# Performance work log

Hardware: AMD Instinct MI355X
Metric: run time of the kernel (lower is better)

The kernel has to match this reference:

```python
import jax, jax.numpy as jnp
import numpy as np

RADIUS = 1.3
COARSE = 32          # coarse_reso
FINE = 2             # fine_reso[0]
NUM_ATOMS = 32
SH_DIM = 9           # (sh_deg+1)^2, sh_deg=2
DATA_DIM = SH_DIM * 3 + 1  # 28
BATCH = 512
N_INT = COARSE * 3 * 2 * FINE  # 384 intersections per ray

# 8 trilinear neighbor offsets, same order as the torch module
_OFFSETS = jnp.array([[-1, -1, -1], [-1, -1, 1], [-1, 1, -1], [-1, 1, 1],
                      [1, -1, -1], [1, -1, 1], [1, 1, -1], [1, 1, 1]], dtype=jnp.float32)


def sh_encode(d):
    """Real spherical harmonics basis, degree 2 (9 components), on normalized dirs."""
    d = d / jnp.linalg.norm(d, axis=-1, keepdims=True)
    x, y, z = d[..., 0], d[..., 1], d[..., 2]
    c0 = 0.28209479177387814
    c1 = 0.48860251190291987
    c2a = 1.0925484305920792
    c2b = 0.31539156525252005
    c2c = 0.5462742152960396
    return jnp.stack([
        c0 * jnp.ones_like(x),
        -c1 * y, c1 * z, -c1 * x,
        c2a * x * y, -c2a * y * z,
        c2b * (2.0 * z * z - x * x - y * y),
        -c2a * x * z,
        c2c * (x * x - y * y)], axis=-1)


def dict_interp(pts, grid, atoms):
    """Multi-res voxel trilinear gather + dictionary-atom accumulate.
    pts: [N,3] world coords; grid: [COARSE^3, A]; atoms: [FINE^3, A, D]."""
    fine_vlen = (2.0 * RADIUS / COARSE) / FINE
    p = (pts + RADIUS) / fine_vlen                       # [N,3] fine-grid coords
    pre = p[:, None, :] + _OFFSETS[None] / 2.0           # [N,8,3]
    post = jnp.clip(jnp.floor(pre), 0.0, COARSE * FINE - 1)
    offs = jnp.abs(p[:, None, :] - (post + 0.5))         # [N,8,3]
    w = jnp.prod(1.0 - offs, axis=-1)                    # [N,8] trilinear weights
    idx = post.astype(jnp.int32)
    c = idx // FINE                                      # coarse cell per-axis
    f = idx % FINE                                       # fine cell per-axis
    cflat = (c[..., 0] * COARSE + c[..., 1]) * COARSE + c[..., 2]  # [N,8]
    fflat = (f[..., 0] * FINE + f[..., 1]) * FINE + f[..., 2]      # [N,8]
    out = jnp.zeros((pts.shape[0], DATA_DIM), pts.dtype)
    for n in range(8):
        cv = grid[cflat[:, n]]                           # [N,A] gathered coarse weights
        av = atoms[fflat[:, n]]                          # [N,A,D] gathered atoms
        out = out + w[:, n, None] * jnp.einsum('na,nad->nd', cv, av)
    return out


def setup_inputs() -> dict:
    key = jax.random.key(0)
    k1, k2, k3, k4 = jax.random.split(key, 4)
    rays_o = jax.random.uniform(k1, (BATCH, 3), jnp.float32, -0.5, 0.5)
    rays_d = jax.random.normal(k2, (BATCH, 3), jnp.float32)
    rays_d = rays_d / jnp.linalg.norm(rays_d, axis=-1, keepdims=True)
    grid = 0.01 * jax.random.normal(k3, (COARSE ** 3, NUM_ATOMS), jnp.float32)
    atoms = jnp.concatenate([
        jax.random.uniform(k4, (FINE ** 3, NUM_ATOMS, DATA_DIM - 1), jnp.float32),
        jnp.full((FINE ** 3, NUM_ATOMS, 1), 0.01, jnp.float32)], axis=-1)
    return {"rays_o": rays_o, "rays_d": rays_d, "grid": grid, "atoms": atoms, "grid_id": 0}


def reference(rays_o, rays_d, grid, atoms, grid_id):
    del grid_id  # single scene
    step = ((2.0 * RADIUS / COARSE) / FINE) / 2.0
    # sample_proposal (no_grad in the original)
    off_pos = (RADIUS - rays_o) / rays_d
    off_neg = (-RADIUS - rays_o) / rays_d
    start = jnp.max(jnp.minimum(off_pos, off_neg), axis=-1, keepdims=True)
    steps = jnp.arange(N_INT, dtype=rays_o.dtype)[None]
    intersections = jax.lax.stop_gradient(start + steps * step)  # [B, N_INT]
    ts = intersections[:, :-1]                                    # [B, S]
    pts = jax.lax.stop_gradient(
        rays_o[:, None, :] + ts[..., None] * rays_d[:, None, :])  # [B,S,3]
    mask = jnp.all((pts > -RADIUS) & (pts < RADIUS), axis=-1)     # [B,S]
    B, S = ts.shape
    data = dict_interp(pts.reshape(-1, 3), grid, atoms).reshape(B, S, DATA_DIM)
    # masked_scatter_ equivalent: zero out out-of-box samples
    sigma = jnp.where(mask, jax.nn.relu(data[..., -1]), 0.0)
    dists = (intersections[:, 1:] - intersections[:, :-1]) * jnp.linalg.norm(rays_d, axis=-1, keepdims=True)
    alpha = 1.0 - jnp.exp(-sigma * dists)
    T = jnp.cumprod(1.0 - alpha + 1e-10, axis=-1)
    T = jnp.concatenate([jnp.ones_like(T[:, :1]), T[:, :-1]], axis=-1)
    abs_light = alpha * T                                         # [B,S]
    sh = sh_encode(rays_d)                                        # [B,SH_DIM]
    sh_vals = data[..., :-1].reshape(B, S, 3, SH_DIM)
    rgb_s = jnp.einsum('bk,bsck->bsc', sh, sh_vals)               # [B,S,3]
    rgb_s = jnp.where(mask[..., None], rgb_s, 0.0)
    rgb = jnp.sum(abs_light[..., None] * jax.nn.sigmoid(rgb_s), axis=1)
    rgb = rgb + (1.0 - jnp.sum(abs_light, axis=-1, keepdims=True))  # white background
    depth = jnp.sum(abs_light * ts, axis=-1)
    consistency_loss = jnp.zeros((), rgb.dtype)  # noise_std == 0
    return rgb, alpha, depth, consistency_loss
```

## Files before the change

### kernel.cpp

```cpp
#include <hip/hip_runtime.h>
#include <math.h>

#define R_ 1.3f
#define NCOARSE 32
#define SAMPLES 383
#define BATCH 512
#define STEPSZ 0.0203125f
#define INV_FINE_VLEN 24.615384615384617f

using f32x4 = __attribute__((ext_vector_type(4))) float;
using s16x8 = __attribute__((ext_vector_type(8))) short;
using u32x4 = __attribute__((ext_vector_type(4))) unsigned int;
using bf16x2 = __attribute__((ext_vector_type(2))) __bf16;

__device__ __forceinline__ unsigned int packbf2(float lo, float hi) {
    bf16x2 v;
    v.x = (__bf16)lo;
    v.y = (__bf16)hi;
    return __builtin_bit_cast(unsigned int, v);
}

__device__ __forceinline__ void dimwc(float p, float* W, int* C) {
    float post0 = fminf(fmaxf(floorf(p - 0.5f), 0.f), 63.f);
    float post1 = fminf(fmaxf(floorf(p + 0.5f), 0.f), 63.f);
    float w0 = 1.f - fabsf(p - (post0 + 0.5f));
    float w1 = 1.f - fabsf(p - (post1 + 0.5f));
    int i0 = (int)post0, i1 = (int)post1;
    int f0 = i0 & 1, f1 = i1 & 1;
    W[0] = (f0 == 0 ? w0 : 0.f) + (f1 == 0 ? w1 : 0.f);
    W[1] = (f0 == 1 ? w0 : 0.f) + (f1 == 1 ? w1 : 0.f);
    int c0 = i0 >> 1, c1 = i1 >> 1;
    C[0] = (f0 == 0) ? c0 : c1;
    C[1] = (f0 == 1) ? c0 : c1;
}

__global__ __launch_bounds__(512, 4) void dp_fused(
    const float* __restrict__ rays_o, const float* __restrict__ rays_d,
    const float* __restrict__ grid, const float* __restrict__ atoms,
    float* __restrict__ out_rgb, float* __restrict__ out_alpha,
    float* __restrict__ out_depth, float* __restrict__ out_loss)
{
    __shared__ u32x4 Bf[16][64];
    __shared__ float Dw[8][544];
    __shared__ float alpha_l[384];
    __shared__ float sig_l[384][3];
    __shared__ float segtot[8];
    __shared__ float part[6][5];

    const int b = blockIdx.x;
    const int tid = threadIdx.x;
    const int wid = tid >> 6, l = tid & 63;
    const int sl = l & 15, j8 = (l >> 4) * 8;

    const int s0i = tid, s1i = tid + 512;
    const int ll0 = s0i & 63, nt0 = (s0i >> 6) & 1, kb0 = s0i >> 7;
    const int ll1 = s1i & 63, nt1 = (s1i >> 6) & 1, kb1 = s1i >> 7;
    const int a00 = (ll0 >> 4) * 8, d0 = nt0 * 16 + (ll0 & 15);
    const int a01 = (ll1 >> 4) * 8, d1 = nt1 * 16 + (ll1 & 15);
    float la0[8], la1[8];
#pragma unroll
    for (int j = 0; j < 8; ++j) {
        la0[j] = (d0 < 28) ? atoms[(kb0 * 32 + a00 + j) * 28 + d0] : 0.f;
        la1[j] = (d1 < 28) ? atoms[(kb1 * 32 + a01 + j) * 28 + d1] : 0.f;
    }

    if (b == 0 && tid == 0) out_loss[0] = 0.f;

    if (tid < 384) alpha_l[tid] = 0.f;
    {
        float* sf = &sig_l[0][0];
        for (int i = tid; i < 384 * 3; i += 512) sf[i] = 0.f;
    }

    const float ox = rays_o[3 * b], oy = rays_o[3 * b + 1], oz = rays_o[3 * b + 2];
    const float dx = rays_d[3 * b], dy = rays_d[3 * b + 1], dz = rays_d[3 * b + 2];
    const float start = fmaxf(fmaxf(
        fminf((R_ - ox) / dx, (-R_ - ox) / dx),
        fminf((R_ - oy) / dy, (-R_ - oy) / dy)),
        fminf((R_ - oz) / dz, (-R_ - oz) / dz));
    const float t_exit = fminf(fminf(
        fmaxf((R_ - ox) / dx, (-R_ - ox) / dx),
        fmaxf((R_ - oy) / dy, (-R_ - oy) / dy)),
        fmaxf((R_ - oz) / dz, (-R_ - oz) / dz));
    const int ns = (int)floorf((t_exit - start) / STEPSZ) + 2;
    const int ntiles = min(24, (ns >> 4) + 2);

    const float lend = sqrtf(dx * dx + dy * dy + dz * dz);
    const float dist = STEPSZ * lend;
    const float inv = 1.f / lend;
    const float nx = dx * inv, ny = dy * inv, nz = dz * inv;
    float sh[9];
    sh[0] = 0.28209479177387814f;
    sh[1] = -0.48860251190291987f * ny;
    sh[2] = 0.48860251190291987f * nz;
    sh[3] = -0.48860251190291987f * nx;
    sh[4] = 1.0925484305920792f * nx * ny;
    sh[5] = -1.0925484305920792f * ny * nz;
    sh[6] = 0.31539156525252005f * (2.f * nz * nz - nx * nx - ny * ny);
    sh[7] = -1.0925484305920792f * nx * nz;
    sh[8] = 0.5462742152960396f * (nx * nx - ny * ny);

    {
        u32x4 o0, o1;
#pragma unroll
        for (int e2 = 0; e2 < 4; ++e2) {
            o0[e2] = packbf2(la0[2 * e2], la0[2 * e2 + 1]);
            o1[e2] = packbf2(la1[2 * e2], la1[2 * e2 + 1]);
        }
        Bf[s0i >> 6][ll0] = o0;
        Bf[s1i >> 6][ll1] = o1;
    }

    __syncthreads();

    float* Dbuf = &Dw[wid][0];

    for (int t = wid; t < ntiles; t += 8) {
        const int s = t * 16 + sl;
        const float tt = start + s * STEPSZ;
        const float px = ox + tt * dx, py = oy + tt * dy, pz = oz + tt * dz;
        const bool m = (s < SAMPLES) &&
                       (px > -R_ && px < R_ && py > -R_ && py < R_ && pz > -R_ && pz < R_);
        if (__ballot(m) == 0ull) continue;

        float W0[2], W1[2], W2[2];
        int C0[2], C1[2], C2[2];
        dimwc((px + R_) * INV_FINE_VLEN, W0, C0);
        dimwc((py + R_) * INV_FINE_VLEN, W1, C1);
        dimwc((pz + R_) * INV_FINE_VLEN, W2, C2);
        const float msk = m ? 1.f : 0.f;

        f32x4 acc0 = {0.f, 0.f, 0.f, 0.f};
        f32x4 acc1 = {0.f, 0.f, 0.f, 0.f};

#pragma unroll
        for (int half = 0; half < 2; ++half) {
            f32x4 qa[4], qb[4];
            float wf[4];
#pragma unroll
            for (int k2 = 0; k2 < 4; ++k2) {
                const int kb = half * 4 + k2;
                const int fx = (kb >> 2) & 1, fy = (kb >> 1) & 1, fz = kb & 1;
                wf[k2] = msk * W0[fx] * W1[fy] * W2[fz];
                const int cf = (C0[fx] * NCOARSE + C1[fy]) * NCOARSE + C2[fz];
                const f32x4* gp = (const f32x4*)(grid + cf * 32 + j8);
                qa[k2] = gp[0];
                qb[k2] = gp[1];
            }
#pragma unroll
            for (int k2 = 0; k2 < 4; ++k2) {
                const int kb = half * 4 + k2;
                const float w = wf[k2];
                u32x4 o;
                o.x = packbf2(w * qa[k2].x, w * qa[k2].y);
                o.y = packbf2(w * qa[k2].z, w * qa[k2].w);
                o.z = packbf2(w * qb[k2].x, w * qb[k2].y);
                o.w = packbf2(w * qb[k2].z, w * qb[k2].w);
                const s16x8 af = __builtin_bit_cast(s16x8, o);
                acc0 = __builtin_amdgcn_mfma_f32_16x16x32_bf16(
                    af, __builtin_bit_cast(s16x8, Bf[kb * 2 + 0][l]), acc0, 0, 0, 0);
                acc1 = __builtin_amdgcn_mfma_f32_16x16x32_bf16(
                    af, __builtin_bit_cast(s16x8, Bf[kb * 2 + 1][l]), acc1, 0, 0, 0);
            }
        }

        const int fp = l >> 4;
#pragma unroll
        for (int r = 0; r < 4; ++r) {
            Dbuf[(4 * fp + r) * 33 + sl]      = acc0[r];
            Dbuf[(4 * fp + r) * 33 + sl + 16] = acc1[r];
        }

        const int s2 = l >> 2, c = l & 3;
        const int so = t * 16 + s2;
        if (c == 3) {
            const float sigma = fmaxf(Dbuf[s2 * 33 + 27], 0.f);
            alpha_l[so] = 1.f - __expf(-sigma * dist);
        } else {
            float r_ = 0.f;
#pragma unroll
            for (int k = 0; k < 9; ++k) r_ += sh[k] * Dbuf[s2 * 33 + c * 9 + k];
            sig_l[so][c] = __builtin_amdgcn_rcpf(1.f + __expf(-r_));
        }
    }

    __syncthreads();

    if (tid < SAMPLES) out_alpha[b * SAMPLES + tid] = alpha_l[tid];

    float a_s = 0.f, incl = 1.f;
    if (wid < 6) {
        const int s = wid * 64 + l;
        const bool v = s < SAMPLES;
        a_s = v ? alpha_l[s] : 0.f;
        incl = v ? (1.f - a_s + 1e-10f) : 1.f;
#pragma unroll
        for (int off = 1; off < 64; off <<= 1) {
            const float tm = __shfl_up(incl, off, 64);
            if (l >= off) incl *= tm;
        }
        if (l == 63) segtot[wid] = incl;
    }
    __syncthreads();
    if (wid < 6) {
        float pre = 1.f;
        for (int k = 0; k < wid; ++k) pre *= segtot[k];
        float excl = __shfl_up(incl, 1, 64);
        if (l == 0) excl = 1.f;
        const int s = wid * 64 + l;
        const bool v = s < SAMPLES;
        const float al = v ? a_s * pre * excl : 0.f;
        float r0 = al * sig_l[s][0];
        float r1 = al * sig_l[s][1];
        float r2 = al * sig_l[s][2];
        float sd = al * (start + s * STEPSZ);
        float sa = al;
#pragma unroll
        for (int m2 = 32; m2 > 0; m2 >>= 1) {
            r0 += __shfl_xor(r0, m2, 64);
            r1 += __shfl_xor(r1, m2, 64);
            r2 += __shfl_xor(r2, m2, 64);
            sd += __shfl_xor(sd, m2, 64);
            sa += __shfl_xor(sa, m2, 64);
        }
        if (l == 0) {
            part[wid][0] = r0; part[wid][1] = r1; part[wid][2] = r2;
            part[wid][3] = sd; part[wid][4] = sa;
        }
    }
    __syncthreads();
    if (tid == 0) {
        float r0 = 0.f, r1 = 0.f, r2 = 0.f, sd = 0.f, sa = 0.f;
#pragma unroll
        for (int j = 0; j < 6; ++j) {
            r0 += part[j][0]; r1 += part[j][1]; r2 += part[j][2];
            sd += part[j][3]; sa += part[j][4];
        }
        const float base = 1.f - sa;
        out_rgb[b * 3 + 0] = r0 + base;
        out_rgb[b * 3 + 1] = r1 + base;
        out_rgb[b * 3 + 2] = r2 + base;
        out_depth[b] = sd;
    }
}

extern "C" void kernel_launch(void* const* d_in, const int* in_sizes, int n_in,
                              void* d_out, int out_size, void* d_ws, size_t ws_size,
                              hipStream_t stream) {
    const float* rays_o = (const float*)d_in[0];
    const float* rays_d = (const float*)d_in[1];
    const float* grid   = (const float*)d_in[2];
    const float* atoms  = (const float*)d_in[3];
    float* out   = (float*)d_out;
    float* rgb   = out;
    float* alpha = out + BATCH * 3;
    float* depth = out + BATCH * 3 + BATCH * SAMPLES;
    float* loss  = out + BATCH * 3 + BATCH * SAMPLES + BATCH;

    dp_fused<<<dim3(BATCH), dim3(512), 0, stream>>>(
        rays_o, rays_d, grid, atoms, rgb, alpha, depth, loss);
}
```

Baseline: 16.99 us.

## Software-pipeline grid gathers across tiles and prefetch before atom barrier

Replaces the per-wave tile loop with an explicitly unrolled, software-pipelined sequence of up to three tiles. The first half of each tile's grid gathers is issued early: the first tile's loads go out before the atom-packing barrier, and the next tile's loads go out while the current tile's MFMAs run. This aims to hide global gather latency. It also drops the per-tile early-skip ballot for fully masked tiles and moves the SH coefficients into shared memory, computed by one thread. That lowers register pressure but adds LDS reads in the epilogue.

```diff
diff --git a/kernel.cpp b/kernel.cpp
--- a/kernel.cpp
+++ b/kernel.cpp
@@ -44,6 +44,7 @@
     __shared__ float Dw[8][544];
     __shared__ float alpha_l[384];
     __shared__ float sig_l[384][3];
+    __shared__ float sh_s[9];
     __shared__ float segtot[8];
     __shared__ float part[6][5];
 
@@ -87,90 +88,73 @@
 
     const float lend = sqrtf(dx * dx + dy * dy + dz * dz);
     const float dist = STEPSZ * lend;
-    const float inv = 1.f / lend;
-    const float nx = dx * inv, ny = dy * inv, nz = dz * inv;
-    float sh[9];
-    sh[0] = 0.28209479177387814f;
-    sh[1] = -0.48860251190291987f * ny;
-    sh[2] = 0.48860251190291987f * nz;
-    sh[3] = -0.48860251190291987f * nx;
-    sh[4] = 1.0925484305920792f * nx * ny;
-    sh[5] = -1.0925484305920792f * ny * nz;
-    sh[6] = 0.31539156525252005f * (2.f * nz * nz - nx * nx - ny * ny);
-    sh[7] = -1.0925484305920792f * nx * nz;
-    sh[8] = 0.5462742152960396f * (nx * nx - ny * ny);
-
-    {
-        u32x4 o0, o1;
-#pragma unroll
-        for (int e2 = 0; e2 < 4; ++e2) {
-            o0[e2] = packbf2(la0[2 * e2], la0[2 * e2 + 1]);
-            o1[e2] = packbf2(la1[2 * e2], la1[2 * e2 + 1]);
-        }
-        Bf[s0i >> 6][ll0] = o0;
-        Bf[s1i >> 6][ll1] = o1;
-    }
-
-    __syncthreads();
-
-    float* Dbuf = &Dw[wid][0];
-
-    for (int t = wid; t < ntiles; t += 8) {
+
+    if (tid == 0) {
+        const float inv = 1.f / lend;
+        const float nx = dx * inv, ny = dy * inv, nz = dz * inv;
+        sh_s[0] = 0.28209479177387814f;
+        sh_s[1] = -0.48860251190291987f * ny;
+        sh_s[2] = 0.48860251190291987f * nz;
+        sh_s[3] = -0.48860251190291987f * nx;
+        sh_s[4] = 1.0925484305920792f * nx * ny;
+        sh_s[5] = -1.0925484305920792f * ny * nz;
+        sh_s[6] = 0.31539156525252005f * (2.f * nz * nz - nx * nx - ny * ny);
+        sh_s[7] = -1.0925484305920792f * nx * nz;
+        sh_s[8] = 0.5462742152960396f * (nx * nx - ny * ny);
+    }
+
+    auto computeWC = [&](int t, float Wx[2], float Wy[2], float Wz[2],
+                         int Cx[2], int Cy[2], int Cz[2]) -> float {
         const int s = t * 16 + sl;
         const float tt = start + s * STEPSZ;
         const float px = ox + tt * dx, py = oy + tt * dy, pz = oz + tt * dz;
         const bool m = (s < SAMPLES) &&
                        (px > -R_ && px < R_ && py > -R_ && py < R_ && pz > -R_ && pz < R_);
-        if (__ballot(m) == 0ull) continue;
-
-        float W0[2], W1[2], W2[2];
-        int C0[2], C1[2], C2[2];
-        dimwc((px + R_) * INV_FINE_VLEN, W0, C0);
-        dimwc((py + R_) * INV_FINE_VLEN, W1, C1);
-        dimwc((pz + R_) * INV_FINE_VLEN, W2, C2);
-        const float msk = m ? 1.f : 0.f;
-
-        f32x4 acc0 = {0.f, 0.f, 0.f, 0.f};
-        f32x4 acc1 = {0.f, 0.f, 0.f, 0.f};
-
-#pragma unroll
-        for (int half = 0; half < 2; ++half) {
-            f32x4 qa[4], qb[4];
-            float wf[4];
-#pragma unroll
-            for (int k2 = 0; k2 < 4; ++k2) {
-                const int kb = half * 4 + k2;
-                const int fx = (kb >> 2) & 1, fy = (kb >> 1) & 1, fz = kb & 1;
-                wf[k2] = msk * W0[fx] * W1[fy] * W2[fz];
-                const int cf = (C0[fx] * NCOARSE + C1[fy]) * NCOARSE + C2[fz];
-                const f32x4* gp = (const f32x4*)(grid + cf * 32 + j8);
-                qa[k2] = gp[0];
-                qb[k2] = gp[1];
-            }
-#pragma unroll
-            for (int k2 = 0; k2 < 4; ++k2) {
-                const int kb = half * 4 + k2;
-                const float w = wf[k2];
-                u32x4 o;
-                o.x = packbf2(w * qa[k2].x, w * qa[k2].y);
-                o.y = packbf2(w * qa[k2].z, w * qa[k2].w);
-                o.z = packbf2(w * qb[k2].x, w * qb[k2].y);
-                o.w = packbf2(w * qb[k2].z, w * qb[k2].w);
-                const s16x8 af = __builtin_bit_cast(s16x8, o);
-                acc0 = __builtin_amdgcn_mfma_f32_16x16x32_bf16(
-                    af, __builtin_bit_cast(s16x8, Bf[kb * 2 + 0][l]), acc0, 0, 0, 0);
-                acc1 = __builtin_amdgcn_mfma_f32_16x16x32_bf16(
-                    af, __builtin_bit_cast(s16x8, Bf[kb * 2 + 1][l]), acc1, 0, 0, 0);
-            }
-        }
-
+        dimwc((px + R_) * INV_FINE_VLEN, Wx, Cx);
+        dimwc((py + R_) * INV_FINE_VLEN, Wy, Cy);
+        dimwc((pz + R_) * INV_FINE_VLEN, Wz, Cz);
+        return m ? 1.f : 0.f;
+    };
+    auto issueHalf = [&](int h, const int Cx[2], const int Cy[2], const int Cz[2],
+                         f32x4 qa[4], f32x4 qb[4]) {
+#pragma unroll
+        for (int k2 = 0; k2 < 4; ++k2) {
+            const int kb = h + k2;
+            const int fx = (kb >> 2) & 1, fy = (kb >> 1) & 1, fz = kb & 1;
+            const int cf = (Cx[fx] * NCOARSE + Cy[fy]) * NCOARSE + Cz[fz];
+            const f32x4* gp = (const f32x4*)(grid + cf * 32 + j8);
+            qa[k2] = gp[0];
+            qb[k2] = gp[1];
+        }
+    };
+    auto consumeHalf = [&](int h, float msk,
+                           const float Wx[2], const float Wy[2], const float Wz[2],
+                           const f32x4 qa[4], const f32x4 qb[4],
+                           f32x4& acc0, f32x4& acc1) {
+#pragma unroll
+        for (int k2 = 0; k2 < 4; ++k2) {
+            const int kb = h + k2;
+            const float w = msk * Wx[(kb >> 2) & 1] * Wy[(kb >> 1) & 1] * Wz[kb & 1];
+            u32x4 o;
+            o.x = packbf2(w * qa[k2].x, w * qa[k2].y);
+            o.y = packbf2(w * qa[k2].z, w * qa[k2].w);
+            o.z = packbf2(w * qb[k2].x, w * qb[k2].y);
+            o.w = packbf2(w * qb[k2].z, w * qb[k2].w);
+            const s16x8 af = __builtin_bit_cast(s16x8, o);
+            acc0 = __builtin_amdgcn_mfma_f32_16x16x32_bf16(
+                af, __builtin_bit_cast(s16x8, Bf[kb * 2 + 0][l]), acc0, 0, 0, 0);
+            acc1 = __builtin_amdgcn_mfma_f32_16x16x32_bf16(
+                af, __builtin_bit_cast(s16x8, Bf[kb * 2 + 1][l]), acc1, 0, 0, 0);
+        }
+    };
+    float* Dbuf = &Dw[wid][0];
+    auto epilogue = [&](int t, const f32x4& acc0, const f32x4& acc1) {
         const int fp = l >> 4;
 #pragma unroll
         for (int r = 0; r < 4; ++r) {
             Dbuf[(4 * fp + r) * 33 + sl]      = acc0[r];
             Dbuf[(4 * fp + r) * 33 + sl + 16] = acc1[r];
         }
-
         const int s2 = l >> 2, c = l & 3;
         const int so = t * 16 + s2;
         if (c == 3) {
@@ -179,8 +163,66 @@
         } else {
             float r_ = 0.f;
 #pragma unroll
-            for (int k = 0; k < 9; ++k) r_ += sh[k] * Dbuf[s2 * 33 + c * 9 + k];
+            for (int k = 0; k < 9; ++k) r_ += sh_s[k] * Dbuf[s2 * 33 + c * 9 + k];
             sig_l[so][c] = __builtin_amdgcn_rcpf(1.f + __expf(-r_));
+        }
+    };
+
+    const bool v0 = wid < ntiles, v1 = wid + 8 < ntiles, v2 = wid + 16 < ntiles;
+
+    float WxA[2], WyA[2], WzA[2], WxB[2], WyB[2], WzB[2];
+    int CxA[2], CyA[2], CzA[2], CxB[2], CyB[2], CzB[2];
+    float mskA = 0.f, mskB = 0.f;
+    f32x4 ga[4], gb[4], ha[4], hb[4];
+
+    if (v0) {
+        mskA = computeWC(wid, WxA, WyA, WzA, CxA, CyA, CzA);
+        issueHalf(0, CxA, CyA, CzA, ga, gb);
+    }
+
+    {
+        u32x4 o0, o1;
+#pragma unroll
+        for (int e2 = 0; e2 < 4; ++e2) {
+            o0[e2] = packbf2(la0[2 * e2], la0[2 * e2 + 1]);
+            o1[e2] = packbf2(la1[2 * e2], la1[2 * e2 + 1]);
+        }
+        Bf[s0i >> 6][ll0] = o0;
+        Bf[s1i >> 6][ll1] = o1;
+    }
+
+    __syncthreads();
+
+    if (v0) {
+        f32x4 acc0 = {0.f, 0.f, 0.f, 0.f};
+        f32x4 acc1 = {0.f, 0.f, 0.f, 0.f};
+        issueHalf(4, CxA, CyA, CzA, ha, hb);
+        consumeHalf(0, mskA, WxA, WyA, WzA, ga, gb, acc0, acc1);
+        if (v1) {
+            mskB = computeWC(wid + 8, WxB, WyB, WzB, CxB, CyB, CzB);
+            issueHalf(0, CxB, CyB, CzB, ga, gb);
+        }
+        consumeHalf(4, mskA, WxA, WyA, WzA, ha, hb, acc0, acc1);
+        epilogue(wid, acc0, acc1);
+        if (v1) {
+            acc0 = {0.f, 0.f, 0.f, 0.f};
+            acc1 = {0.f, 0.f, 0.f, 0.f};
+            issueHalf(4, CxB, CyB, CzB, ha, hb);
+            consumeHalf(0, mskB, WxB, WyB, WzB, ga, gb, acc0, acc1);
+            if (v2) {
+                mskA = computeWC(wid + 16, WxA, WyA, WzA, CxA, CyA, CzA);
+                issueHalf(0, CxA, CyA, CzA, ga, gb);
+            }
+            consumeHalf(4, mskB, WxB, WyB, WzB, ha, hb, acc0, acc1);
+            epilogue(wid + 8, acc0, acc1);
+            if (v2) {
+                acc0 = {0.f, 0.f, 0.f, 0.f};
+                acc1 = {0.f, 0.f, 0.f, 0.f};
+                issueHalf(4, CxA, CyA, CzA, ha, hb);
+                consumeHalf(0, mskA, WxA, WyA, WzA, ga, gb, acc0, acc1);
+                consumeHalf(4, mskA, WxA, WyA, WzA, ha, hb, acc0, acc1);
+                epilogue(wid + 16, acc0, acc1);
+            }
         }
     }
 
```

Measured after the change: 29.32 us. 1.73x slower.
